# Kernel optimization log

Measured on AMD Instinct MI355X. Metric: run time of the kernel, lower is better.

## Reference

```python
import jax, jax.numpy as jnp
import numpy as np

M, K, N = 32, 8192, 8192      # tokens, infeatures, outfeatures
GROUP = 128                   # quantization group size along K
PACK = 8                      # 32 bits / 4 bits per value


def _dequant(qweight, scales):
    """Unpack int4 nibbles (packed 8-per-int32 along K) and apply per-group
    symmetric dequant: w = (q - 8) * scale, matching Marlin's fused dequant."""
    kp, n = qweight.shape  # (K//8, N)
    shifts = (4 * jnp.arange(PACK, dtype=jnp.int32))[None, :, None]
    q = ((qweight[:, None, :] >> shifts) & 15)          # (K//8, 8, N)
    q = q.reshape(kp * PACK, n).astype(jnp.float32)     # (K, N)
    groups = scales.shape[0]
    gsz = (kp * PACK) // groups
    w = (q.reshape(groups, gsz, n) - 8.0) * scales[:, None, :]
    return w.reshape(kp * PACK, n)                      # (K, N) fp


def setup_inputs() -> dict:
    key = jax.random.key(0)
    kA, kQ, kS, kB = jax.random.split(key, 4)
    A = jax.random.normal(kA, (M, K), jnp.float32)
    # draw raw 4-bit codes then pack 8 of them into each int32 along K
    q4 = jax.random.randint(kQ, (K, N), 0, 16, jnp.int32)
    shifts = (4 * jnp.arange(PACK, dtype=jnp.int32))[None, :, None]
    qweight = jnp.sum(q4.reshape(K // PACK, PACK, N) << shifts, axis=1).astype(jnp.int32)
    scales = jax.random.uniform(kS, (K // GROUP, N), jnp.float32, 0.005, 0.02)
    bias = jax.random.normal(kB, (N,), jnp.float32) * 0.01
    return {"A": A, "qweight": qweight, "scales": scales, "bias": bias}


def reference(A, qweight, scales, bias):
    # Marlin mul(A, B, C, s) computes C = A @ dequant(B, s); then + bias
    W = _dequant(qweight, scales)          # (K, N)
    return A @ W + bias                    # (M, N)
```

## Files before the change

kernel.cpp:

```cpp
#include <hip/hip_runtime.h>
#include <hip/hip_bf16.h>
#include <stdint.h>

#define M_DIM 32
#define K_DIM 8192
#define N_DIM 8192
#define NGROUPS 64
#define GSZ 128
#define KSPLIT 4
#define KPART (K_DIM / KSPLIT)
#define GPART (NGROUPS / KSPLIT)
#define BN 64

typedef __attribute__((ext_vector_type(8))) short short8;
typedef __attribute__((ext_vector_type(4))) float floatx4;

__global__ void marlin_prep_kernel(const float* __restrict__ A,
                                   uint16_t* __restrict__ Abf,
                                   float* __restrict__ R,
                                   float4* __restrict__ out4) {
    const int m = blockIdx.x;
    const int qtr = blockIdx.y;
    const int t = threadIdx.x;
    const int octet = qtr * 256 + t;
    const int k0 = octet * 8;

    {
        const int gtid = (qtr * 32 + m) * 256 + t;
        const float4 z = make_float4(0.f, 0.f, 0.f, 0.f);
        out4[gtid * 2] = z;
        out4[gtid * 2 + 1] = z;
    }

    const float* a = A + m * K_DIM + k0;
    uint16_t b[8];
    float sum = 0.f;
#pragma unroll
    for (int j = 0; j < 8; j++) {
        union { __hip_bfloat16 h; uint16_t u; } cv;
        cv.h = __float2bfloat16(a[j]);
        b[j] = cv.u;
        sum += __bfloat162float(cv.h);
    }
    uint32_t w0 = (uint32_t)b[0] | ((uint32_t)b[4] << 16);
    uint32_t w1 = (uint32_t)b[1] | ((uint32_t)b[5] << 16);
    uint32_t w2 = (uint32_t)b[2] | ((uint32_t)b[6] << 16);
    uint32_t w3 = (uint32_t)b[3] | ((uint32_t)b[7] << 16);
    uint4 packed = make_uint4(w0, w1, w2, w3);
    *(uint4*)(Abf + (size_t)m * K_DIM + k0) = packed;

#pragma unroll
    for (int off = 1; off < 16; off <<= 1) sum += __shfl_xor(sum, off, 16);
    if ((t & 15) == 0) R[m * NGROUPS + qtr * 16 + (t >> 4)] = sum;
}

__global__ __launch_bounds__(512, 4) void
MarlinQuantLinear_68556267979256_kernel(const int* __restrict__ qw,
                                        const float* __restrict__ scales,
                                        const float* __restrict__ bias,
                                        const uint16_t* __restrict__ Abf,
                                        const float* __restrict__ R,
                                        float* __restrict__ out) {
    __shared__ float r_lds[32 * 17];

    const int bx = blockIdx.x;
    const int bz = blockIdx.y;
    const int nbase = bx * BN;
    const int kbase = bz * KPART;
    const int gbase = bz * GPART;

    const int tid = threadIdx.x;
    const int w = tid >> 6;
    const int lane = tid & 63;
    const int quad = lane >> 4;
    const int l16 = lane & 15;
    const int mtile = w & 1;
    const int ntile = w >> 1;
    const int ncol = nbase + ntile * 16 + l16;

    {
        const int mm = tid >> 4, gg = tid & 15;
        r_lds[mm * 17 + gg] = 136.0f * R[mm * NGROUPS + gbase + gg];
    }
    __syncthreads();

    const uint16_t* arow = Abf + (size_t)(mtile * 16 + l16) * K_DIM
                               + kbase + quad * 8;
    const int* qcol = qw + (size_t)(kbase >> 3) * N_DIM + ncol;
    const float* scol = scales + (size_t)gbase * N_DIM + ncol;

    floatx4 C = {0.f, 0.f, 0.f, 0.f};

#pragma unroll 2
    for (int g = 0; g < GPART; g++) {
        const float s = scol[g * N_DIM];
        floatx4 accg = {0.f, 0.f, 0.f, 0.f};
#pragma unroll
        for (int t = 0; t < 4; t++) {
            const uint32_t q = (uint32_t)qcol[(g * 16 + t * 4 + quad) * N_DIM];
            union { uint32_t u[4]; short8 v; } fb;
            fb.u[0] = ( q        & 0x000F000Fu) | 0x43004300u;
            fb.u[1] = ((q >> 4)  & 0x000F000Fu) | 0x43004300u;
            fb.u[2] = ((q >> 8)  & 0x000F000Fu) | 0x43004300u;
            fb.u[3] = ((q >> 12) & 0x000F000Fu) | 0x43004300u;
            const short8 fa = *(const short8*)(arow + g * 128 + t * 32);
            accg = __builtin_amdgcn_mfma_f32_16x16x32_bf16(fa, fb.v, accg, 0, 0, 0);
        }
#pragma unroll
        for (int r = 0; r < 4; r++) {
            const float tval = accg[r] - r_lds[(mtile * 16 + quad * 4 + r) * 17 + g];
            C[r] = fmaf(s, tval, C[r]);
        }
    }

    const float bv = (bz == 0) ? bias[ncol] : 0.0f;
#pragma unroll
    for (int r = 0; r < 4; r++) {
        const int m = mtile * 16 + quad * 4 + r;
        atomicAdd(&out[(size_t)m * N_DIM + ncol], C[r] + bv);
    }
}

extern "C" void kernel_launch(void* const* d_in, const int* in_sizes, int n_in,
                              void* d_out, int out_size, void* d_ws, size_t ws_size,
                              hipStream_t stream) {
    const float* A      = (const float*)d_in[0];
    const int*   qw     = (const int*)d_in[1];
    const float* scales = (const float*)d_in[2];
    const float* bias   = (const float*)d_in[3];
    float* out = (float*)d_out;

    uint16_t* Abf = (uint16_t*)d_ws;
    float*    R   = (float*)((char*)d_ws + (size_t)M_DIM * K_DIM * 2);

    marlin_prep_kernel<<<dim3(M_DIM, 4), 256, 0, stream>>>(A, Abf, R, (float4*)out);
    MarlinQuantLinear_68556267979256_kernel<<<dim3(N_DIM / BN, KSPLIT), 512, 0, stream>>>(
        qw, scales, bias, Abf, R, out);
}
```

Measured before the change: 112.3 us.

## Double K-split and preload all weight/scale loads into registers with A prefetch

Raises the K split from 4 to 8, which doubles the grid to 1024 blocks and halves the per-block K range. Each thread now issues all of its packed-weight and scale loads for its slice up front into registers. It also software-pipelines the bf16 activation loads one group ahead, so more memory requests are in flight and latency is hidden better. In exchange, register pressure rises and atomic adds into the output double.

```diff
diff --git a/kernel.cpp b/kernel.cpp
--- a/kernel.cpp
+++ b/kernel.cpp
@@ -7,7 +7,7 @@
 #define N_DIM 8192
 #define NGROUPS 64
 #define GSZ 128
-#define KSPLIT 4
+#define KSPLIT 8
 #define KPART (K_DIM / KSPLIT)
 #define GPART (NGROUPS / KSPLIT)
 #define BN 64
@@ -61,7 +61,7 @@
                                         const uint16_t* __restrict__ Abf,
                                         const float* __restrict__ R,
                                         float* __restrict__ out) {
-    __shared__ float r_lds[32 * 17];
+    __shared__ float r_lds[32 * 9];
 
     const int bx = blockIdx.x;
     const int bz = blockIdx.y;
@@ -78,38 +78,61 @@
     const int ntile = w >> 1;
     const int ncol = nbase + ntile * 16 + l16;
 
-    {
-        const int mm = tid >> 4, gg = tid & 15;
-        r_lds[mm * 17 + gg] = 136.0f * R[mm * NGROUPS + gbase + gg];
+    if (tid < 256) {
+        const int mm = tid >> 3, gg = tid & 7;
+        r_lds[mm * 9 + gg] = 136.0f * R[mm * NGROUPS + gbase + gg];
     }
     __syncthreads();
 
+    const float* scol = scales + (size_t)gbase * N_DIM + ncol;
+    float s[GPART];
+#pragma unroll
+    for (int g = 0; g < GPART; g++) s[g] = scol[g * N_DIM];
+
+    const int* qcol = qw + (size_t)(kbase >> 3) * N_DIM + ncol;
+    uint32_t qv[GPART][4];
+#pragma unroll
+    for (int g = 0; g < GPART; g++)
+#pragma unroll
+        for (int t = 0; t < 4; t++)
+            qv[g][t] = (uint32_t)qcol[(g * 16 + t * 4 + quad) * N_DIM];
+
     const uint16_t* arow = Abf + (size_t)(mtile * 16 + l16) * K_DIM
                                + kbase + quad * 8;
-    const int* qcol = qw + (size_t)(kbase >> 3) * N_DIM + ncol;
-    const float* scol = scales + (size_t)gbase * N_DIM + ncol;
+    short8 a_cur[4];
+#pragma unroll
+    for (int t = 0; t < 4; t++)
+        a_cur[t] = *(const short8*)(arow + t * 32);
 
     floatx4 C = {0.f, 0.f, 0.f, 0.f};
 
-#pragma unroll 2
+#pragma unroll
     for (int g = 0; g < GPART; g++) {
-        const float s = scol[g * N_DIM];
+        short8 a_nxt[4];
+        if (g + 1 < GPART) {
+#pragma unroll
+            for (int t = 0; t < 4; t++)
+                a_nxt[t] = *(const short8*)(arow + (g + 1) * 128 + t * 32);
+        }
         floatx4 accg = {0.f, 0.f, 0.f, 0.f};
 #pragma unroll
         for (int t = 0; t < 4; t++) {
-            const uint32_t q = (uint32_t)qcol[(g * 16 + t * 4 + quad) * N_DIM];
+            const uint32_t q = qv[g][t];
             union { uint32_t u[4]; short8 v; } fb;
             fb.u[0] = ( q        & 0x000F000Fu) | 0x43004300u;
             fb.u[1] = ((q >> 4)  & 0x000F000Fu) | 0x43004300u;
             fb.u[2] = ((q >> 8)  & 0x000F000Fu) | 0x43004300u;
             fb.u[3] = ((q >> 12) & 0x000F000Fu) | 0x43004300u;
-            const short8 fa = *(const short8*)(arow + g * 128 + t * 32);
-            accg = __builtin_amdgcn_mfma_f32_16x16x32_bf16(fa, fb.v, accg, 0, 0, 0);
+            accg = __builtin_amdgcn_mfma_f32_16x16x32_bf16(a_cur[t], fb.v, accg, 0, 0, 0);
         }
 #pragma unroll
         for (int r = 0; r < 4; r++) {
-            const float tval = accg[r] - r_lds[(mtile * 16 + quad * 4 + r) * 17 + g];
-            C[r] = fmaf(s, tval, C[r]);
+            const float tval = accg[r] - r_lds[(mtile * 16 + quad * 4 + r) * 9 + g];
+            C[r] = fmaf(s[g], tval, C[r]);
+        }
+        if (g + 1 < GPART) {
+#pragma unroll
+            for (int t = 0; t < 4; t++) a_cur[t] = a_nxt[t];
         }
     }
 
```

After: 109.7 us. 1.02x faster.

## Stage weights and activations through double-buffered LDS with async global-to-LDS loads

Applied to the files above, without the earlier changes.

The main GEMM loop stops reading packed int4 weights and bf16 activations straight from global memory. It now stages each group's tiles into double-buffered shared memory using global_load_lds, with XOR swizzles to avoid bank conflicts, and prefetches the next group while the current one is computed. All per-group scales are also hoisted into registers before the loop. The aim is to overlap memory latency with MFMA work and to share A loads across the warps of a block, at the cost of more LDS use, a barrier every iteration, and higher register pressure from full unrolling.

```diff
diff --git a/kernel.cpp b/kernel.cpp
--- a/kernel.cpp
+++ b/kernel.cpp
@@ -6,7 +6,6 @@
 #define K_DIM 8192
 #define N_DIM 8192
 #define NGROUPS 64
-#define GSZ 128
 #define KSPLIT 4
 #define KPART (K_DIM / KSPLIT)
 #define GPART (NGROUPS / KSPLIT)
@@ -14,6 +13,9 @@
 
 typedef __attribute__((ext_vector_type(8))) short short8;
 typedef __attribute__((ext_vector_type(4))) float floatx4;
+
+#define AS1(p) ((const __attribute__((address_space(1))) void*)(p))
+#define AS3(p) ((__attribute__((address_space(3))) void*)(p))
 
 __global__ void marlin_prep_kernel(const float* __restrict__ A,
                                    uint16_t* __restrict__ Abf,
@@ -46,8 +48,7 @@
     uint32_t w1 = (uint32_t)b[1] | ((uint32_t)b[5] << 16);
     uint32_t w2 = (uint32_t)b[2] | ((uint32_t)b[6] << 16);
     uint32_t w3 = (uint32_t)b[3] | ((uint32_t)b[7] << 16);
-    uint4 packed = make_uint4(w0, w1, w2, w3);
-    *(uint4*)(Abf + (size_t)m * K_DIM + k0) = packed;
+    *(uint4*)(Abf + (size_t)m * K_DIM + k0) = make_uint4(w0, w1, w2, w3);
 
 #pragma unroll
     for (int off = 1; off < 16; off <<= 1) sum += __shfl_xor(sum, off, 16);
@@ -61,13 +62,16 @@
                                         const uint16_t* __restrict__ Abf,
                                         const float* __restrict__ R,
                                         float* __restrict__ out) {
-    __shared__ float r_lds[32 * 17];
+    __shared__ uint32_t qbuf[2][16 * 64];
+    __shared__ uint32_t abuf[2][32 * 64];
+    __shared__ float    r_lds[32 * 17];
 
     const int bx = blockIdx.x;
     const int bz = blockIdx.y;
     const int nbase = bx * BN;
     const int kbase = bz * KPART;
     const int gbase = bz * GPART;
+    const int qrow0 = bz * (KPART / 8);
 
     const int tid = threadIdx.x;
     const int w = tid >> 6;
@@ -77,39 +81,62 @@
     const int mtile = w & 1;
     const int ntile = w >> 1;
     const int ncol = nbase + ntile * 16 + l16;
+    const int arow = mtile * 16 + l16;
 
     {
         const int mm = tid >> 4, gg = tid & 15;
         r_lds[mm * 17 + gg] = 136.0f * R[mm * NGROUPS + gbase + gg];
     }
-    __syncthreads();
 
-    const uint16_t* arow = Abf + (size_t)(mtile * 16 + l16) * K_DIM
-                               + kbase + quad * 8;
-    const int* qcol = qw + (size_t)(kbase >> 3) * N_DIM + ncol;
     const float* scol = scales + (size_t)gbase * N_DIM + ncol;
+    float s[GPART];
+#pragma unroll
+    for (int g = 0; g < GPART; g++) s[g] = scol[g * N_DIM];
+
+    const int sra = tid >> 4, spa = tid & 15;
+    const uint16_t* ga_base = Abf + (size_t)sra * K_DIM + kbase
+                            + ((spa ^ (sra & 15)) << 3);
+    const int srq = tid >> 4, spq = tid & 15;
+    const int* gq_base = qw + (size_t)(qrow0 + srq) * N_DIM + nbase
+                       + ((spq * 4) ^ ((srq & 1) << 4));
+
+    auto stage = [&](int g, int buf) {
+        __builtin_amdgcn_global_load_lds(AS1(ga_base + g * 128),
+                                         AS3(&abuf[buf][w * 256]), 16, 0, 0);
+        if (tid < 256)
+            __builtin_amdgcn_global_load_lds(AS1(gq_base + (size_t)g * 16 * N_DIM),
+                                             AS3(&qbuf[buf][w * 256]), 16, 0, 0);
+    };
+
+    stage(0, 0);
 
     floatx4 C = {0.f, 0.f, 0.f, 0.f};
 
-#pragma unroll 2
+#pragma unroll
     for (int g = 0; g < GPART; g++) {
-        const float s = scol[g * N_DIM];
+        __syncthreads();
+        if (g + 1 < GPART) stage(g + 1, (g + 1) & 1);
+
+        const uint32_t* qb = qbuf[g & 1];
+        const uint32_t* ab = abuf[g & 1];
         floatx4 accg = {0.f, 0.f, 0.f, 0.f};
 #pragma unroll
         for (int t = 0; t < 4; t++) {
-            const uint32_t q = (uint32_t)qcol[(g * 16 + t * 4 + quad) * N_DIM];
+            const uint32_t q =
+                qb[(t * 4 + quad) * 64 + ((ntile * 16 + l16) ^ ((quad & 1) << 4))];
             union { uint32_t u[4]; short8 v; } fb;
             fb.u[0] = ( q        & 0x000F000Fu) | 0x43004300u;
             fb.u[1] = ((q >> 4)  & 0x000F000Fu) | 0x43004300u;
             fb.u[2] = ((q >> 8)  & 0x000F000Fu) | 0x43004300u;
             fb.u[3] = ((q >> 12) & 0x000F000Fu) | 0x43004300u;
-            const short8 fa = *(const short8*)(arow + g * 128 + t * 32);
+            const short8 fa = *(const short8*)
+                &ab[arow * 64 + (((t * 4 + quad) ^ (arow & 15)) << 2)];
             accg = __builtin_amdgcn_mfma_f32_16x16x32_bf16(fa, fb.v, accg, 0, 0, 0);
         }
 #pragma unroll
         for (int r = 0; r < 4; r++) {
             const float tval = accg[r] - r_lds[(mtile * 16 + quad * 4 + r) * 17 + g];
-            C[r] = fmaf(s, tval, C[r]);
+            C[r] = fmaf(s[g], tval, C[r]);
         }
     }
 
```

Result: faster. 107.5 us (-4.3%).
